# Optimization experiments

Measured on AMD Instinct MI355X. Metric: run time of the kernel, lower is better.

Reference implementation:

```python
import jax, jax.numpy as jnp
import numpy as np

N, H, W = 4, 96, 96
C, G, K = 128, 8, 3
GC = C // G          # group channels = 16
P = K * K            # sampling points per group = 9
PAD = K // 2
OFS = 1.0            # offset_scale
HID = 4 * C          # mlp hidden
EPS = 1e-5           # torch nn.LayerNorm default eps


def _ln(x, g, b):
    m = jnp.mean(x, -1, keepdims=True)
    v = jnp.mean((x - m) ** 2, -1, keepdims=True)
    return (x - m) * jax.lax.rsqrt(v + EPS) * g + b


def _dcnv3_core(x, offset, mask):
    # x: (n,H,W,C) channels-last, offset: (n,H,W,G*P*2), mask: (n,H,W,G,P) softmaxed.
    # Faithful port of dcnv3_core_pytorch (stride=1, dilation=1, zero-pad grid_sample,
    # align_corners=False -> pixel = loc*size - 0.5).
    n = x.shape[0]
    xp = jnp.pad(x, ((0, 0), (PAD, PAD), (PAD, PAD), (0, 0)))
    Hin, Win = H + 2 * PAD, W + 2 * PAD
    L = H * W
    base = (K - 1) // 2 + 0.5
    ref_x = (base + jnp.arange(W, dtype=x.dtype)) / Win  # normalized by padded size
    ref_y = (base + jnp.arange(H, dtype=x.dtype)) / Hin
    k = jnp.arange(K, dtype=x.dtype) - (K - 1) // 2
    dx = jnp.repeat(k, K) / Win  # torch meshgrid('ij'): kernel-x varies slowest
    dy = jnp.tile(k, K) / Hin
    off = offset.reshape(n, H, W, G, P, 2)
    # absolute sampling pixel coords (grid_sample align_corners=False)
    px = (ref_x[None, None, :, None, None] + dx * OFS + off[..., 0] * OFS / Win) * Win - 0.5
    py = (ref_y[None, :, None, None, None] + dy * OFS + off[..., 1] * OFS / Hin) * Hin - 0.5
    # layout (n,G,L,P)
    px = px.transpose(0, 3, 1, 2, 4).reshape(n, G, L, P)
    py = py.transpose(0, 3, 1, 2, 4).reshape(n, G, L, P)
    mk = mask.transpose(0, 3, 1, 2, 4).reshape(n, G, L, P)
    xg = xp.reshape(n, Hin * Win, G, GC).transpose(0, 2, 1, 3)
    x0 = jnp.floor(px); y0 = jnp.floor(py)
    fx = px - x0; fy = py - y0
    x0 = x0.astype(jnp.int32); y0 = y0.astype(jnp.int32)
    x1 = x0 + 1; y1 = y0 + 1
    out = jnp.zeros((n, G, L, GC), x.dtype)
    for yi, xi, w in ((y0, x0, (1 - fy) * (1 - fx)), (y0, x1, (1 - fy) * fx),
                      (y1, x0, fy * (1 - fx)), (y1, x1, fy * fx)):
        valid = (yi >= 0) & (yi < Hin) & (xi >= 0) & (xi < Win)
        idx = jnp.clip(yi, 0, Hin - 1) * Win + jnp.clip(xi, 0, Win - 1)
        v = jnp.take_along_axis(xg, idx.reshape(n, G, L * P, 1), axis=2)
        v = v.reshape(n, G, L, P, GC)
        out = out + jnp.einsum('nglp,nglpc->nglc', jnp.where(valid, w, 0.0) * mk, v)
    return out.transpose(0, 2, 1, 3).reshape(n, H, W, C)


def _dcn(x, w_in, b_in, dw_k, dw_b, dwg, dwb, w_off, b_off, w_msk, b_msk, w_out, b_out):
    n = x.shape[0]
    xproj = x @ w_in + b_in
    x1 = jax.lax.conv_general_dilated(
        x, dw_k, (1, 1), 'SAME',
        dimension_numbers=('NHWC', 'HWIO', 'NHWC'),
        feature_group_count=C) + dw_b
    x1 = jax.nn.gelu(_ln(x1, dwg, dwb), approximate=False)
    offset = x1 @ w_off + b_off
    mask = jax.nn.softmax((x1 @ w_msk + b_msk).reshape(n, H, W, G, P), axis=-1)
    y = _dcnv3_core(xproj, offset, mask)
    return y @ w_out + b_out


def setup_inputs() -> dict:
    key = jax.random.key(0)
    ks = jax.random.split(key, 10)
    rn = lambda k, s, sc: jax.random.normal(k, s, jnp.float32) * sc
    return {
        'x': rn(ks[0], (N, H, W, C), 1.0),
        'ln1g': jnp.ones((C,), jnp.float32), 'ln1b': jnp.zeros((C,), jnp.float32),
        'w_in': rn(ks[1], (C, C), 0.02), 'b_in': jnp.zeros((C,), jnp.float32),
        'dw_k': rn(ks[2], (K, K, 1, C), 0.1), 'dw_b': jnp.zeros((C,), jnp.float32),
        'dwg': jnp.ones((C,), jnp.float32), 'dwb': jnp.zeros((C,), jnp.float32),
        'w_off': rn(ks[3], (C, G * P * 2), 0.01), 'b_off': rn(ks[4], (G * P * 2,), 0.1),
        'w_msk': rn(ks[5], (C, G * P), 0.02), 'b_msk': jnp.zeros((G * P,), jnp.float32),
        'w_out': rn(ks[6], (C, C), 0.02), 'b_out': jnp.zeros((C,), jnp.float32),
        'ln2g': jnp.ones((C,), jnp.float32), 'ln2b': jnp.zeros((C,), jnp.float32),
        'w1': rn(ks[7], (C, HID), 0.02), 'b1': jnp.zeros((HID,), jnp.float32),
        'w2': rn(ks[8], (HID, C), 0.02), 'b2': jnp.zeros((C,), jnp.float32),
    }


def reference(x, ln1g, ln1b, w_in, b_in, dw_k, dw_b, dwg, dwb, w_off, b_off,
              w_msk, b_msk, w_out, b_out, ln2g, ln2b, w1, b1, w2, b2):
    # pre-norm InternImage block: x = x + dcn(LN1(x)); x = x + mlp(LN2(x))
    x = x + _dcn(_ln(x, ln1g, ln1b), w_in, b_in, dw_k, dw_b, dwg, dwb,
                 w_off, b_off, w_msk, b_msk, w_out, b_out)
    h = _ln(x, ln2g, ln2b)
    h = jax.nn.gelu(h @ w1 + b1, approximate=False) @ w2 + b2
    return x + h
```

## Files before the change

### kernel.cpp

```cpp
#include <hip/hip_runtime.h>
#include <hip/hip_bf16.h>
#include <math.h>

using bf16 = __hip_bfloat16;
using bf162 = __hip_bfloat162;

typedef __bf16 bf16x8 __attribute__((ext_vector_type(8)));
typedef float floatx4 __attribute__((ext_vector_type(4)));

constexpr int NB = 4, HH = 96, WW = 96, CC = 128, GG = 8, PP = 9;
constexpr int HW = HH * WW;
constexpr int NPIX = NB * HW;

__device__ __forceinline__ float ld1(const float* p) { return *p; }
__device__ __forceinline__ float ld1(const bf16* p)  { return __bfloat162float(*p); }
__device__ __forceinline__ void st1(float* p, float v) { *p = v; }
__device__ __forceinline__ void st1(bf16* p, float v)  { *p = __float2bfloat16(v); }
__device__ __forceinline__ float b2f(bf16 v) { return __bfloat162float(v); }
__device__ __forceinline__ bf16 f2b(float v) { return __float2bfloat16(v); }
__device__ __forceinline__ float gelu_exact(float v) {
    return 0.5f * v * (1.0f + erff(v * 0.7071067811865475f));
}
__device__ __forceinline__ floatx4 MFMA(bf16x8 a, bf16x8 b, floatx4 c) {
    return __builtin_amdgcn_mfma_f32_16x16x32_bf16(a, b, c, 0, 0, 0);
}

struct PrepArgs {
    const float* src[6];
    bf16* dst[6];
    int K[6], N[6];
    int cum[7];
    const float* b_off; const float* b_msk; float* b_om;
};

__global__ __launch_bounds__(256) void prep_weights(PrepArgs pa, int total)
{
    int t = blockIdx.x * 256 + threadIdx.x;
    if (t >= total) return;
    if (t >= pa.cum[6]) {
        int e = t - pa.cum[6];
        pa.b_om[e] = (e < 144) ? pa.b_off[e] : pa.b_msk[e - 144];
        return;
    }
    int i = 0;
    #pragma unroll
    for (int j = 0; j < 5; ++j) if (t >= pa.cum[j + 1]) i = j + 1;
    int e = t - pa.cum[i];
    int Ki = pa.K[i], Ni = pa.N[i];
    int n = e / Ki, k = e - n * Ki;
    pa.dst[i][e] = f2b(pa.src[i][(size_t)k * Ni + n]);
}

template<typename TI, typename TO>
__global__ __launch_bounds__(256) void ln_kernel(
    const TI* __restrict__ X, const float* __restrict__ g,
    const float* __restrict__ b, TO* __restrict__ out)
{
    int wave = (blockIdx.x * 256 + threadIdx.x) >> 6;
    int lane = threadIdx.x & 63;
    if (wave >= NPIX) return;
    const TI* xp = X + (size_t)wave * 128 + 2 * lane;
    float v0 = ld1(xp), v1 = ld1(xp + 1);
    float s = v0 + v1, q = v0 * v0 + v1 * v1;
    #pragma unroll
    for (int o = 32; o; o >>= 1) { s += __shfl_xor(s, o); q += __shfl_xor(q, o); }
    float mean = s * (1.0f / 128.0f);
    float rstd = rsqrtf(q * (1.0f / 128.0f) - mean * mean + 1e-5f);
    float g0 = g[2 * lane], g1 = g[2 * lane + 1];
    float b0 = b[2 * lane], b1 = b[2 * lane + 1];
    TO* op = out + (size_t)wave * 128 + 2 * lane;
    st1(op,     (v0 - mean) * rstd * g0 + b0);
    st1(op + 1, (v1 - mean) * rstd * g1 + b1);
}

__global__ __launch_bounds__(256) void dwconv_ln_gelu_kernel(
    const bf16* __restrict__ xln, const float* __restrict__ dwk,
    const float* __restrict__ dwb, const float* __restrict__ gam,
    const float* __restrict__ bet, bf16* __restrict__ out)
{
    int wave = (blockIdx.x * 256 + threadIdx.x) >> 6;
    int lane = threadIdx.x & 63;
    if (wave >= NPIX) return;
    int n = wave / HW; int rem = wave % HW;
    int y = rem / WW;  int x = rem % WW;
    const bf162* xp = (const bf162*)xln;
    float a0 = 0.f, a1 = 0.f;
    #pragma unroll
    for (int ky = 0; ky < 3; ++ky) {
        int yy = y + ky - 1;
        if (yy < 0 || yy >= HH) continue;
        #pragma unroll
        for (int kx = 0; kx < 3; ++kx) {
            int xx = x + kx - 1;
            if (xx < 0 || xx >= WW) continue;
            bf162 v = xp[((size_t)(n * HH + yy) * WW + xx) * 64 + lane];
            const float* w = dwk + (ky * 3 + kx) * CC + 2 * lane;
            a0 = fmaf(b2f(v.x), w[0], a0);
            a1 = fmaf(b2f(v.y), w[1], a1);
        }
    }
    a0 += dwb[2 * lane]; a1 += dwb[2 * lane + 1];
    float s = a0 + a1, q = a0 * a0 + a1 * a1;
    #pragma unroll
    for (int o = 32; o; o >>= 1) { s += __shfl_xor(s, o); q += __shfl_xor(q, o); }
    float mean = s * (1.0f / 128.0f);
    float rstd = rsqrtf(q * (1.0f / 128.0f) - mean * mean + 1e-5f);
    float h0 = gelu_exact((a0 - mean) * rstd * gam[2 * lane]     + bet[2 * lane]);
    float h1 = gelu_exact((a1 - mean) * rstd * gam[2 * lane + 1] + bet[2 * lane + 1]);
    bf162 o2; o2.x = f2b(h0); o2.y = f2b(h1);
    ((bf162*)out)[(size_t)wave * 64 + lane] = o2;
}

__global__ __launch_bounds__(256) void dcn_core_kernel(
    const bf16* __restrict__ xproj, const bf16* __restrict__ omr,
    bf16* __restrict__ out)
{
    __shared__ int4   sOff[4][72];
    __shared__ float4 sW[4][72];
    __shared__ float  sRaw[4][72];
    int wv = threadIdx.x >> 6;
    int lane = threadIdx.x & 63;
    int pix = blockIdx.x * 4 + wv;
    int n = pix / HW; int rem = pix % HW;
    int iy = rem / WW; int ix = rem % WW;
    const bf16* om = omr + (size_t)pix * 216;

    for (int e = lane; e < 72; e += 64)
        sRaw[wv][e] = b2f(om[144 + e]);
    __syncthreads();

    for (int e = lane; e < 72; e += 64) {
        int g = e / 9, p = e - 9 * g;
        float mx = -1e30f;
        #pragma unroll
        for (int i = 0; i < 9; ++i) mx = fmaxf(mx, sRaw[wv][g * 9 + i]);
        float ssum = 0.f;
        #pragma unroll
        for (int i = 0; i < 9; ++i) ssum += __expf(sRaw[wv][g * 9 + i] - mx);
        float mw = __expf(sRaw[wv][e] - mx) / ssum;

        float ox = b2f(om[g * 18 + 2 * p]);
        float oy = b2f(om[g * 18 + 2 * p + 1]);
        int kx = p / 3 - 1, ky = p % 3 - 1;
        float px = (float)(ix + kx) + ox;
        float py = (float)(iy + ky) + oy;
        float fx0 = floorf(px), fy0 = floorf(py);
        int x0 = (int)fx0, y0 = (int)fy0;
        float fx = px - fx0, fy = py - fy0;
        bool vx0 = (x0 >= 0) & (x0 < WW), vx1 = (x0 + 1 >= 0) & (x0 + 1 < WW);
        bool vy0 = (y0 >= 0) & (y0 < HH), vy1 = (y0 + 1 >= 0) & (y0 + 1 < HH);
        float w00 = (1.f - fy) * (1.f - fx) * mw * (vy0 && vx0 ? 1.f : 0.f);
        float w01 = (1.f - fy) * fx         * mw * (vy0 && vx1 ? 1.f : 0.f);
        float w10 = fy * (1.f - fx)         * mw * (vy1 && vx0 ? 1.f : 0.f);
        float w11 = fy * fx                 * mw * (vy1 && vx1 ? 1.f : 0.f);
        int x0c = min(max(x0, 0), WW - 1), x1c = min(max(x0 + 1, 0), WW - 1);
        int y0c = min(max(y0, 0), HH - 1), y1c = min(max(y0 + 1, 0), HH - 1);
        sOff[wv][e] = make_int4((y0c * WW + x0c) * CC, (y0c * WW + x1c) * CC,
                                (y1c * WW + x0c) * CC, (y1c * WW + x1c) * CC);
        sW[wv][e] = make_float4(w00, w01, w10, w11);
    }
    __syncthreads();

    const bf16* xb = xproj + (size_t)n * HW * CC + 2 * lane;
    int gbase = (lane >> 3) * 9;
    float a0 = 0.f, a1 = 0.f;
    #pragma unroll
    for (int p = 0; p < 9; ++p) {
        int4 o = sOff[wv][gbase + p];
        float4 w = sW[wv][gbase + p];
        bf162 v00 = *(const bf162*)(xb + o.x);
        bf162 v01 = *(const bf162*)(xb + o.y);
        bf162 v10 = *(const bf162*)(xb + o.z);
        bf162 v11 = *(const bf162*)(xb + o.w);
        a0 += w.x * b2f(v00.x) + w.y * b2f(v01.x) + w.z * b2f(v10.x) + w.w * b2f(v11.x);
        a1 += w.x * b2f(v00.y) + w.y * b2f(v01.y) + w.z * b2f(v10.y) + w.w * b2f(v11.y);
    }
    bf162 o2; o2.x = f2b(a0); o2.y = f2b(a1);
    ((bf162*)out)[(size_t)pix * 64 + lane] = o2;
}

__global__ __launch_bounds__(256) void gemm_mfma_kernel(
    const bf16* __restrict__ A, const bf16* __restrict__ Wt,
    const float* __restrict__ bias, bf16* __restrict__ Out, int M, int Nn, int K)
{
    __shared__ __align__(16) __bf16 As[64][72];
    __shared__ __align__(16) __bf16 Bs[64][72];
    int tid = threadIdx.x;
    int wv = tid >> 6, lane = tid & 63;
    int bm = blockIdx.y * 64, bn = blockIdx.x * 64;
    int mI = lane & 15, q = lane >> 4;
    floatx4 acc[4] = {};

    for (int k0 = 0; k0 < K; k0 += 64) {
        #pragma unroll
        for (int cc = 0; cc < 2; ++cc) {
            int ch = tid * 2 + cc;
            int row = ch >> 3, ko = (ch & 7) * 8;
            *reinterpret_cast<uint4*>(&As[row][ko]) =
                *reinterpret_cast<const uint4*>(A + (size_t)(bm + row) * K + k0 + ko);
            int ng = bn + row;
            uint4 bv = make_uint4(0, 0, 0, 0);
            if (ng < Nn) bv = *reinterpret_cast<const uint4*>(Wt + (size_t)ng * K + k0 + ko);
            *reinterpret_cast<uint4*>(&Bs[row][ko]) = bv;
        }
        __syncthreads();
        #pragma unroll
        for (int kk = 0; kk < 64; kk += 32) {
            bf16x8 a = *reinterpret_cast<const bf16x8*>(&As[wv * 16 + mI][kk + q * 8]);
            #pragma unroll
            for (int t = 0; t < 4; ++t) {
                bf16x8 b = *reinterpret_cast<const bf16x8*>(&Bs[t * 16 + mI][kk + q * 8]);
                acc[t] = MFMA(a, b, acc[t]);
            }
        }
        __syncthreads();
    }
    int row0 = bm + wv * 16 + q * 4;
    #pragma unroll
    for (int t = 0; t < 4; ++t) {
        int col = bn + t * 16 + mI;
        if (col >= Nn) continue;
        float bs = bias[col];
        #pragma unroll
        for (int r = 0; r < 4; ++r)
            st1(Out + (size_t)(row0 + r) * Nn + col, acc[t][r] + bs);
    }
}

__global__ __launch_bounds__(256, 3) void fused_tail_kernel(
    const bf16* __restrict__ ycore, const float* __restrict__ x,
    const bf16* __restrict__ w_outT, const float* __restrict__ b_out,
    const float* __restrict__ ln2g, const float* __restrict__ ln2b,
    const bf16* __restrict__ w1T, const float* __restrict__ b1,
    const bf16* __restrict__ w2T, const float* __restrict__ b2,
    float* __restrict__ out)
{
    __shared__ __align__(16) bf16 sA[64 * 136];
    __shared__ __align__(16) bf16 sXres[64 * 136];
    __shared__ __align__(16) bf16 sH2[64 * 136];
    int tid = threadIdx.x, wv = tid >> 6, lane = tid & 63;
    int mI = lane & 15, q = lane >> 4;
    int bm = blockIdx.x * 64;

    bf16x8 bw0[4][2];
    #pragma unroll
    for (int ks = 0; ks < 4; ++ks)
        #pragma unroll
        for (int ct = 0; ct < 2; ++ct)
            bw0[ks][ct] = *reinterpret_cast<const bf16x8*>(
                w_outT + (size_t)(wv * 32 + ct * 16 + mI) * 128 + ks * 32 + q * 8);

    #pragma unroll
    for (int i = 0; i < 4; ++i) {
        int s = tid + 256 * i;
        int row = s >> 4, ko = (s & 15) * 8;
        *reinterpret_cast<uint4*>(&sA[row * 136 + ko]) =
            *reinterpret_cast<const uint4*>(ycore + (size_t)(bm + row) * 128 + ko);
    }
    __syncthreads();

    floatx4 acc0[4][2] = {};
    #pragma unroll
    for (int ks = 0; ks < 4; ++ks) {
        int k = ks * 32 + q * 8;
        bf16x8 a[4];
        #pragma unroll
        for (int rt = 0; rt < 4; ++rt)
            a[rt] = *reinterpret_cast<const bf16x8*>(&sA[(rt * 16 + mI) * 136 + k]);
        #pragma unroll
        for (int ct = 0; ct < 2; ++ct)
            #pragma unroll
            for (int rt = 0; rt < 4; ++rt)
                acc0[rt][ct] = MFMA(a[rt], bw0[ks][ct], acc0[rt][ct]);
    }
    #pragma unroll
    for (int rt = 0; rt < 4; ++rt)
        #pragma unroll
        for (int ct = 0; ct < 2; ++ct) {
            int col = wv * 32 + ct * 16 + mI;
            float bs = b_out[col];
            #pragma unroll
            for (int r = 0; r < 4; ++r) {
                int row = rt * 16 + q * 4 + r;
                float v = acc0[rt][ct][r] + bs + x[(size_t)(bm + row) * 128 + col];
                sXres[row * 136 + col] = f2b(v);
            }
        }
    __syncthreads();

    {
        int row = tid >> 2, part = tid & 3;
        float s = 0.f, sq = 0.f;
        float vals[32];
        #pragma unroll
        for (int j = 0; j < 4; ++j) {
            bf16x8 v = *reinterpret_cast<const bf16x8*>(&sXres[row * 136 + part * 32 + j * 8]);
            #pragma unroll
            for (int e = 0; e < 8; ++e) {
                float f = (float)v[e];
                vals[j * 8 + e] = f; s += f; sq += f * f;
            }
        }
        s  += __shfl_xor(s, 1);  s += __shfl_xor(s, 2);
        sq += __shfl_xor(sq, 1); sq += __shfl_xor(sq, 2);
        float mean = s * (1.0f / 128.0f);
        float rstd = rsqrtf(sq * (1.0f / 128.0f) - mean * mean + 1e-5f);
        #pragma unroll
        for (int j = 0; j < 4; ++j) {
            bf16x8 o;
            #pragma unroll
            for (int e = 0; e < 8; ++e) {
                int ch = part * 32 + j * 8 + e;
                bf16 t = f2b((vals[j * 8 + e] - mean) * rstd * ln2g[ch] + ln2b[ch]);
                o[e] = *reinterpret_cast<__bf16*>(&t);
            }
            *reinterpret_cast<bf16x8*>(&sH2[row * 136 + part * 32 + j * 8]) = o;
        }
    }
    __syncthreads();

    floatx4 acc2[4][2] = {};
    #pragma unroll 1
    for (int ph = 0; ph < 4; ++ph) {
        bf16x8 bw1[4][2];
        #pragma unroll
        for (int ks = 0; ks < 4; ++ks)
            #pragma unroll
            for (int ct = 0; ct < 2; ++ct)
                bw1[ks][ct] = *reinterpret_cast<const bf16x8*>(
                    w1T + (size_t)(ph * 128 + wv * 32 + ct * 16 + mI) * 128 + ks * 32 + q * 8);
        floatx4 acc1[4][2] = {};
        #pragma unroll
        for (int ks = 0; ks < 4; ++ks) {
            int k = ks * 32 + q * 8;
            bf16x8 a[4];
            #pragma unroll
            for (int rt = 0; rt < 4; ++rt)
                a[rt] = *reinterpret_cast<const bf16x8*>(&sH2[(rt * 16 + mI) * 136 + k]);
            #pragma unroll
            for (int ct = 0; ct < 2; ++ct)
                #pragma unroll
                for (int rt = 0; rt < 4; ++rt)
                    acc1[rt][ct] = MFMA(a[rt], bw1[ks][ct], acc1[rt][ct]);
        }
        __syncthreads();
        bf16x8 bw2[4][2];
        #pragma unroll
        for (int ks = 0; ks < 4; ++ks)
            #pragma unroll
            for (int ct = 0; ct < 2; ++ct)
                bw2[ks][ct] = *reinterpret_cast<const bf16x8*>(
                    w2T + (size_t)(wv * 32 + ct * 16 + mI) * 512 + ph * 128 + ks * 32 + q * 8);
        #pragma unroll
        for (int rt = 0; rt < 4; ++rt)
            #pragma unroll
            for (int ct = 0; ct < 2; ++ct) {
                int lcol = wv * 32 + ct * 16 + mI;
                float bs = b1[ph * 128 + lcol];
                #pragma unroll
                for (int r = 0; r < 4; ++r) {
                    int row = rt * 16 + q * 4 + r;
                    sA[row * 136 + lcol] = f2b(gelu_exact(acc1[rt][ct][r] + bs));
                }
            }
        __syncthreads();
        #pragma unroll
        for (int ks = 0; ks < 4; ++ks) {
            int k = ks * 32 + q * 8;
            bf16x8 a[4];
            #pragma unroll
            for (int rt = 0; rt < 4; ++rt)
                a[rt] = *reinterpret_cast<const bf16x8*>(&sA[(rt * 16 + mI) * 136 + k]);
            #pragma unroll
            for (int ct = 0; ct < 2; ++ct)
                #pragma unroll
                for (int rt = 0; rt < 4; ++rt)
                    acc2[rt][ct] = MFMA(a[rt], bw2[ks][ct], acc2[rt][ct]);
        }
    }
    #pragma unroll
    for (int rt = 0; rt < 4; ++rt)
        #pragma unroll
        for (int ct = 0; ct < 2; ++ct) {
            int col = wv * 32 + ct * 16 + mI;
            float bs = b2[col];
            #pragma unroll
            for (int r = 0; r < 4; ++r) {
                int row = rt * 16 + q * 4 + r;
                out[(size_t)(bm + row) * 128 + col] =
                    acc2[rt][ct][r] + bs + b2f(sXres[row * 136 + col]);
            }
        }
}

extern "C" void kernel_launch(void* const* d_in, const int* in_sizes, int n_in,
                              void* d_out, int out_size, void* d_ws, size_t ws_size,
                              hipStream_t stream)
{
    const float* x     = (const float*)d_in[0];
    const float* ln1g  = (const float*)d_in[1];
    const float* ln1b  = (const float*)d_in[2];
    const float* w_in  = (const float*)d_in[3];
    const float* b_in  = (const float*)d_in[4];
    const float* dw_k  = (const float*)d_in[5];
    const float* dw_b  = (const float*)d_in[6];
    const float* dwg   = (const float*)d_in[7];
    const float* dwb   = (const float*)d_in[8];
    const float* w_off = (const float*)d_in[9];
    const float* b_off = (const float*)d_in[10];
    const float* w_msk = (const float*)d_in[11];
    const float* b_msk = (const float*)d_in[12];
    const float* w_out = (const float*)d_in[13];
    const float* b_out = (const float*)d_in[14];
    const float* ln2g  = (const float*)d_in[15];
    const float* ln2b  = (const float*)d_in[16];
    const float* w1    = (const float*)d_in[17];
    const float* b1    = (const float*)d_in[18];
    const float* w2    = (const float*)d_in[19];
    const float* b2    = (const float*)d_in[20];
    float* out = (float*)d_out;

    bf16* ws = (bf16*)d_ws;
    bf16* xln   = ws;
    bf16* xproj = xln   + (size_t)NPIX * 128;
    bf16* x1    = xproj + (size_t)NPIX * 128;
    bf16* omr   = x1    + (size_t)NPIX * 128;
    bf16* ycore = xln;
    bf16* wT    = ws + (size_t)NPIX * 600;
    bf16* w_inT  = wT;
    bf16* w_omT  = w_inT  + 16384;
    bf16* w_outT = w_omT  + 27648;
    bf16* w1T    = w_outT + 16384;
    bf16* w2T    = w1T    + 65536;
    float* b_om  = (float*)(w2T + 65536);
    const int WTOT = 191488 + 216;

    PrepArgs pa;
    pa.src[0] = w_in;  pa.dst[0] = w_inT;            pa.K[0] = 128; pa.N[0] = 128;
    pa.src[1] = w_off; pa.dst[1] = w_omT;            pa.K[1] = 128; pa.N[1] = 144;
    pa.src[2] = w_msk; pa.dst[2] = w_omT + 144*128;  pa.K[2] = 128; pa.N[2] = 72;
    pa.src[3] = w_out; pa.dst[3] = w_outT;           pa.K[3] = 128; pa.N[3] = 128;
    pa.src[4] = w1;    pa.dst[4] = w1T;              pa.K[4] = 128; pa.N[4] = 512;
    pa.src[5] = w2;    pa.dst[5] = w2T;              pa.K[5] = 512; pa.N[5] = 128;
    pa.cum[0] = 0;     pa.cum[1] = 16384;  pa.cum[2] = 34816; pa.cum[3] = 44032;
    pa.cum[4] = 60416; pa.cum[5] = 125952; pa.cum[6] = 191488;
    pa.b_off = b_off;  pa.b_msk = b_msk;   pa.b_om = b_om;

    const int M = NPIX;
    dim3 blk(256);

    prep_weights<<<(WTOT + 255) / 256, blk, 0, stream>>>(pa, WTOT);
    ln_kernel<float, bf16><<<NPIX / 4, blk, 0, stream>>>(x, ln1g, ln1b, xln);
    gemm_mfma_kernel<<<dim3(2, M / 64), blk, 0, stream>>>(
        xln, w_inT, b_in, xproj, M, 128, 128);
    dwconv_ln_gelu_kernel<<<NPIX / 4, blk, 0, stream>>>(xln, dw_k, dw_b, dwg, dwb, x1);
    gemm_mfma_kernel<<<dim3(4, M / 64), blk, 0, stream>>>(
        x1, w_omT, b_om, omr, M, 216, 128);
    dcn_core_kernel<<<NPIX / 4, blk, 0, stream>>>(xproj, omr, ycore);
    fused_tail_kernel<<<M / 64, blk, 0, stream>>>(
        ycore, x, w_outT, b_out, ln2g, ln2b, w1T, b1, w2T, b2, out);
}
```

Baseline: 236.9 us.

## Replace exact GELU with tanh approximation and keep LN2 residual in registers

Swaps the erf-based GELU for a tanh-form approximation written as a sigmoid with __expf, both in the depthwise-conv kernel and in the MLP tail. In the fused tail kernel the residual is now kept in accumulator registers rather than an LDS buffer. LayerNorm statistics are reduced with shuffles plus a small per-wave partial-sum array, which removes the sXres shared array. Launch bounds go from 3 to 4 blocks per SM to exploit the lower LDS footprint, at the cost of register pressure and a small numerical deviation from exact GELU.

```diff
diff --git a/kernel.cpp b/kernel.cpp
--- a/kernel.cpp
+++ b/kernel.cpp
@@ -18,8 +18,10 @@
 __device__ __forceinline__ void st1(bf16* p, float v)  { *p = __float2bfloat16(v); }
 __device__ __forceinline__ float b2f(bf16 v) { return __bfloat162float(v); }
 __device__ __forceinline__ bf16 f2b(float v) { return __float2bfloat16(v); }
-__device__ __forceinline__ float gelu_exact(float v) {
-    return 0.5f * v * (1.0f + erff(v * 0.7071067811865475f));
+__device__ __forceinline__ float gelu_fast(float v) {
+    float p = v * v;
+    float u2 = v * (-1.5957691216f - 0.0713548162f * p);
+    return v / (1.0f + __expf(u2));
 }
 __device__ __forceinline__ floatx4 MFMA(bf16x8 a, bf16x8 b, floatx4 c) {
     return __builtin_amdgcn_mfma_f32_16x16x32_bf16(a, b, c, 0, 0, 0);
@@ -105,8 +107,8 @@
     for (int o = 32; o; o >>= 1) { s += __shfl_xor(s, o); q += __shfl_xor(q, o); }
     float mean = s * (1.0f / 128.0f);
     float rstd = rsqrtf(q * (1.0f / 128.0f) - mean * mean + 1e-5f);
-    float h0 = gelu_exact((a0 - mean) * rstd * gam[2 * lane]     + bet[2 * lane]);
-    float h1 = gelu_exact((a1 - mean) * rstd * gam[2 * lane + 1] + bet[2 * lane + 1]);
+    float h0 = gelu_fast((a0 - mean) * rstd * gam[2 * lane]     + bet[2 * lane]);
+    float h1 = gelu_fast((a1 - mean) * rstd * gam[2 * lane + 1] + bet[2 * lane + 1]);
     bf162 o2; o2.x = f2b(h0); o2.y = f2b(h1);
     ((bf162*)out)[(size_t)wave * 64 + lane] = o2;
 }
@@ -227,7 +229,7 @@
     }
 }
 
-__global__ __launch_bounds__(256, 3) void fused_tail_kernel(
+__global__ __launch_bounds__(256, 4) void fused_tail_kernel(
     const bf16* __restrict__ ycore, const float* __restrict__ x,
     const bf16* __restrict__ w_outT, const float* __restrict__ b_out,
     const float* __restrict__ ln2g, const float* __restrict__ ln2b,
@@ -236,8 +238,9 @@
     float* __restrict__ out)
 {
     __shared__ __align__(16) bf16 sA[64 * 136];
-    __shared__ __align__(16) bf16 sXres[64 * 136];
     __shared__ __align__(16) bf16 sH2[64 * 136];
+    __shared__ __align__(16) float sPS[64][4];
+    __shared__ __align__(16) float sPQ[64][4];
     int tid = threadIdx.x, wv = tid >> 6, lane = tid & 63;
     int mI = lane & 15, q = lane >> 4;
     int bm = blockIdx.x * 64;
@@ -249,6 +252,12 @@
         for (int ct = 0; ct < 2; ++ct)
             bw0[ks][ct] = *reinterpret_cast<const bf16x8*>(
                 w_outT + (size_t)(wv * 32 + ct * 16 + mI) * 128 + ks * 32 + q * 8);
+    float g2[2], be2[2];
+    #pragma unroll
+    for (int ct = 0; ct < 2; ++ct) {
+        int col = wv * 32 + ct * 16 + mI;
+        g2[ct] = ln2g[col]; be2[ct] = ln2b[col];
+    }
 
     #pragma unroll
     for (int i = 0; i < 4; ++i) {
@@ -274,7 +283,10 @@
                 acc0[rt][ct] = MFMA(a[rt], bw0[ks][ct], acc0[rt][ct]);
     }
     #pragma unroll
-    for (int rt = 0; rt < 4; ++rt)
+    for (int rt = 0; rt < 4; ++rt) {
+        float ps[4], pq[4];
+        #pragma unroll
+        for (int r = 0; r < 4; ++r) { ps[r] = 0.f; pq[r] = 0.f; }
         #pragma unroll
         for (int ct = 0; ct < 2; ++ct) {
             int col = wv * 32 + ct * 16 + mI;
@@ -283,40 +295,42 @@
             for (int r = 0; r < 4; ++r) {
                 int row = rt * 16 + q * 4 + r;
                 float v = acc0[rt][ct][r] + bs + x[(size_t)(bm + row) * 128 + col];
-                sXres[row * 136 + col] = f2b(v);
-            }
-        }
+                v = b2f(f2b(v));
+                acc0[rt][ct][r] = v;
+                ps[r] += v; pq[r] += v * v;
+            }
+        }
+        #pragma unroll
+        for (int r = 0; r < 4; ++r) {
+            #pragma unroll
+            for (int o = 1; o < 16; o <<= 1) {
+                ps[r] += __shfl_xor(ps[r], o);
+                pq[r] += __shfl_xor(pq[r], o);
+            }
+            int row = rt * 16 + q * 4 + r;
+            if (mI == 0) { sPS[row][wv] = ps[r]; sPQ[row][wv] = pq[r]; }
+        }
+    }
     __syncthreads();
 
-    {
-        int row = tid >> 2, part = tid & 3;
-        float s = 0.f, sq = 0.f;
-        float vals[32];
-        #pragma unroll
-        for (int j = 0; j < 4; ++j) {
-            bf16x8 v = *reinterpret_cast<const bf16x8*>(&sXres[row * 136 + part * 32 + j * 8]);
-            #pragma unroll
-            for (int e = 0; e < 8; ++e) {
-                float f = (float)v[e];
-                vals[j * 8 + e] = f; s += f; sq += f * f;
-            }
-        }
-        s  += __shfl_xor(s, 1);  s += __shfl_xor(s, 2);
-        sq += __shfl_xor(sq, 1); sq += __shfl_xor(sq, 2);
-        float mean = s * (1.0f / 128.0f);
-        float rstd = rsqrtf(sq * (1.0f / 128.0f) - mean * mean + 1e-5f);
-        #pragma unroll
-        for (int j = 0; j < 4; ++j) {
-            bf16x8 o;
-            #pragma unroll
-            for (int e = 0; e < 8; ++e) {
-                int ch = part * 32 + j * 8 + e;
-                bf16 t = f2b((vals[j * 8 + e] - mean) * rstd * ln2g[ch] + ln2b[ch]);
-                o[e] = *reinterpret_cast<__bf16*>(&t);
-            }
-            *reinterpret_cast<bf16x8*>(&sH2[row * 136 + part * 32 + j * 8]) = o;
-        }
-    }
+    #pragma unroll
+    for (int rt = 0; rt < 4; ++rt)
+        #pragma unroll
+        for (int r = 0; r < 4; ++r) {
+            int row = rt * 16 + q * 4 + r;
+            float4 s4 = *reinterpret_cast<const float4*>(&sPS[row][0]);
+            float4 q4 = *reinterpret_cast<const float4*>(&sPQ[row][0]);
+            float s = s4.x + s4.y + s4.z + s4.w;
+            float sq = q4.x + q4.y + q4.z + q4.w;
+            float mean = s * (1.0f / 128.0f);
+            float rstd = rsqrtf(sq * (1.0f / 128.0f) - mean * mean + 1e-5f);
+            #pragma unroll
+            for (int ct = 0; ct < 2; ++ct) {
+                int col = wv * 32 + ct * 16 + mI;
+                sH2[row * 136 + col] =
+                    f2b((acc0[rt][ct][r] - mean) * rstd * g2[ct] + be2[ct]);
+            }
+        }
     __syncthreads();
 
     floatx4 acc2[4][2] = {};
@@ -360,7 +374,7 @@
                 #pragma unroll
                 for (int r = 0; r < 4; ++r) {
                     int row = rt * 16 + q * 4 + r;
-                    sA[row * 136 + lcol] = f2b(gelu_exact(acc1[rt][ct][r] + bs));
+                    sA[row * 136 + lcol] = f2b(gelu_fast(acc1[rt][ct][r] + bs));
                 }
             }
         __syncthreads();
@@ -388,7 +402,7 @@
             for (int r = 0; r < 4; ++r) {
                 int row = rt * 16 + q * 4 + r;
                 out[(size_t)(bm + row) * 128 + col] =
-                    acc2[rt][ct][r] + bs + b2f(sXres[row * 136 + col]);
+                    acc2[rt][ct][r] + bs + acc0[rt][ct][r];
             }
         }
 }
```

After: 250.0 us. 5.5% more time.

## Fuse LayerNorm into input-projection GEMM and use tanh-form GELU approximation

Applied to the files above, without the earlier changes.

Removes the standalone LayerNorm kernel and computes LN1 inside the first GEMM's prologue, writing the normalized activations to global for the depthwise conv and also straight into shared memory for the MFMA. The GEMM now loads the full K=128 tile in one pass with a padded 136-stride layout instead of two 64-wide iterations. Exact erf GELU is replaced with a sigmoid-form tanh approximation using __expf in both the dwconv and MLP paths. Both grid.x blocks of the fused kernel redundantly recompute the LayerNorm and store xln twice, and the GELU change alters numerics.

```diff
diff --git a/kernel.cpp b/kernel.cpp
--- a/kernel.cpp
+++ b/kernel.cpp
@@ -18,8 +18,10 @@
 __device__ __forceinline__ void st1(bf16* p, float v)  { *p = __float2bfloat16(v); }
 __device__ __forceinline__ float b2f(bf16 v) { return __bfloat162float(v); }
 __device__ __forceinline__ bf16 f2b(float v) { return __float2bfloat16(v); }
-__device__ __forceinline__ float gelu_exact(float v) {
-    return 0.5f * v * (1.0f + erff(v * 0.7071067811865475f));
+__device__ __forceinline__ float gelu_fast(float v) {
+    float p = v * v;
+    float u2 = v * (-1.5957691216f - 0.0713548162f * p);
+    return v / (1.0f + __expf(u2));
 }
 __device__ __forceinline__ floatx4 MFMA(bf16x8 a, bf16x8 b, floatx4 c) {
     return __builtin_amdgcn_mfma_f32_16x16x32_bf16(a, b, c, 0, 0, 0);
@@ -51,26 +53,89 @@
     pa.dst[i][e] = f2b(pa.src[i][(size_t)k * Ni + n]);
 }
 
-template<typename TI, typename TO>
-__global__ __launch_bounds__(256) void ln_kernel(
-    const TI* __restrict__ X, const float* __restrict__ g,
-    const float* __restrict__ b, TO* __restrict__ out)
-{
-    int wave = (blockIdx.x * 256 + threadIdx.x) >> 6;
-    int lane = threadIdx.x & 63;
-    if (wave >= NPIX) return;
-    const TI* xp = X + (size_t)wave * 128 + 2 * lane;
-    float v0 = ld1(xp), v1 = ld1(xp + 1);
-    float s = v0 + v1, q = v0 * v0 + v1 * v1;
-    #pragma unroll
-    for (int o = 32; o; o >>= 1) { s += __shfl_xor(s, o); q += __shfl_xor(q, o); }
-    float mean = s * (1.0f / 128.0f);
-    float rstd = rsqrtf(q * (1.0f / 128.0f) - mean * mean + 1e-5f);
-    float g0 = g[2 * lane], g1 = g[2 * lane + 1];
-    float b0 = b[2 * lane], b1 = b[2 * lane + 1];
-    TO* op = out + (size_t)wave * 128 + 2 * lane;
-    st1(op,     (v0 - mean) * rstd * g0 + b0);
-    st1(op + 1, (v1 - mean) * rstd * g1 + b1);
+template<bool DOLN>
+__global__ __launch_bounds__(256) void lngemm_kernel(
+    const void* __restrict__ Ain, const bf16* __restrict__ Wt,
+    const float* __restrict__ bias,
+    const float* __restrict__ lng, const float* __restrict__ lnb,
+    bf16* __restrict__ xlnOut,
+    bf16* __restrict__ Out, int Nn)
+{
+    __shared__ __align__(16) bf16 As[64 * 136];
+    __shared__ __align__(16) bf16 Bs[64 * 136];
+    int tid = threadIdx.x, wv = tid >> 6, lane = tid & 63;
+    int mI = lane & 15, q = lane >> 4;
+    int bm = blockIdx.y * 64, bn = blockIdx.x * 64;
+
+    if (DOLN) {
+        int row = tid >> 2, seg = tid & 3;
+        const float* rp = (const float*)Ain + (size_t)(bm + row) * 128 + seg * 32;
+        float v[32]; float s = 0.f, sq = 0.f;
+        #pragma unroll
+        for (int j = 0; j < 8; ++j) {
+            float4 f = *reinterpret_cast<const float4*>(rp + j * 4);
+            v[j*4+0] = f.x; v[j*4+1] = f.y; v[j*4+2] = f.z; v[j*4+3] = f.w;
+            s += f.x + f.y + f.z + f.w;
+            sq += f.x*f.x + f.y*f.y + f.z*f.z + f.w*f.w;
+        }
+        s  += __shfl_xor(s, 1);  s += __shfl_xor(s, 2);
+        sq += __shfl_xor(sq, 1); sq += __shfl_xor(sq, 2);
+        float mean = s * (1.0f / 128.0f);
+        float rstd = rsqrtf(sq * (1.0f / 128.0f) - mean * mean + 1e-5f);
+        bf16x8 o[4];
+        #pragma unroll
+        for (int j = 0; j < 32; ++j) {
+            int ch = seg * 32 + j;
+            bf16 tb = f2b((v[j] - mean) * rstd * lng[ch] + lnb[ch]);
+            o[j >> 3][j & 7] = *reinterpret_cast<__bf16*>(&tb);
+        }
+        #pragma unroll
+        for (int j = 0; j < 4; ++j) {
+            *reinterpret_cast<bf16x8*>(&As[row * 136 + seg * 32 + j * 8]) = o[j];
+            *reinterpret_cast<bf16x8*>(xlnOut + (size_t)(bm + row) * 128 + seg * 32 + j * 8) = o[j];
+        }
+    } else {
+        const bf16* A = (const bf16*)Ain;
+        #pragma unroll
+        for (int i = 0; i < 4; ++i) {
+            int sI = tid + 256 * i;
+            int row = sI >> 4, ko = (sI & 15) * 8;
+            *reinterpret_cast<uint4*>(&As[row * 136 + ko]) =
+                *reinterpret_cast<const uint4*>(A + (size_t)(bm + row) * 128 + ko);
+        }
+    }
+    #pragma unroll
+    for (int i = 0; i < 4; ++i) {
+        int sI = tid + 256 * i;
+        int row = sI >> 4, ko = (sI & 15) * 8;
+        int ng = bn + row;
+        uint4 bv = make_uint4(0, 0, 0, 0);
+        if (ng < Nn) bv = *reinterpret_cast<const uint4*>(Wt + (size_t)ng * 128 + ko);
+        *reinterpret_cast<uint4*>(&Bs[row * 136 + ko]) = bv;
+    }
+    __syncthreads();
+
+    floatx4 acc[4] = {};
+    #pragma unroll
+    for (int kk = 0; kk < 4; ++kk) {
+        int k = kk * 32 + q * 8;
+        bf16x8 a = *reinterpret_cast<const bf16x8*>(&As[(wv * 16 + mI) * 136 + k]);
+        #pragma unroll
+        for (int t = 0; t < 4; ++t) {
+            bf16x8 b = *reinterpret_cast<const bf16x8*>(&Bs[(t * 16 + mI) * 136 + k]);
+            acc[t] = MFMA(a, b, acc[t]);
+        }
+    }
+    int row0 = bm + wv * 16 + q * 4;
+    #pragma unroll
+    for (int t = 0; t < 4; ++t) {
+        int col = bn + t * 16 + mI;
+        if (col >= Nn) continue;
+        float bs = bias[col];
+        #pragma unroll
+        for (int r = 0; r < 4; ++r)
+            st1(Out + (size_t)(row0 + r) * Nn + col, acc[t][r] + bs);
+    }
 }
 
 __global__ __launch_bounds__(256) void dwconv_ln_gelu_kernel(
@@ -105,8 +170,8 @@
     for (int o = 32; o; o >>= 1) { s += __shfl_xor(s, o); q += __shfl_xor(q, o); }
     float mean = s * (1.0f / 128.0f);
     float rstd = rsqrtf(q * (1.0f / 128.0f) - mean * mean + 1e-5f);
-    float h0 = gelu_exact((a0 - mean) * rstd * gam[2 * lane]     + bet[2 * lane]);
-    float h1 = gelu_exact((a1 - mean) * rstd * gam[2 * lane + 1] + bet[2 * lane + 1]);
+    float h0 = gelu_fast((a0 - mean) * rstd * gam[2 * lane]     + bet[2 * lane]);
+    float h1 = gelu_fast((a1 - mean) * rstd * gam[2 * lane + 1] + bet[2 * lane + 1]);
     bf162 o2; o2.x = f2b(h0); o2.y = f2b(h1);
     ((bf162*)out)[(size_t)wave * 64 + lane] = o2;
 }
@@ -179,54 +244,6 @@
     ((bf162*)out)[(size_t)pix * 64 + lane] = o2;
 }
 
-__global__ __launch_bounds__(256) void gemm_mfma_kernel(
-    const bf16* __restrict__ A, const bf16* __restrict__ Wt,
-    const float* __restrict__ bias, bf16* __restrict__ Out, int M, int Nn, int K)
-{
-    __shared__ __align__(16) __bf16 As[64][72];
-    __shared__ __align__(16) __bf16 Bs[64][72];
-    int tid = threadIdx.x;
-    int wv = tid >> 6, lane = tid & 63;
-    int bm = blockIdx.y * 64, bn = blockIdx.x * 64;
-    int mI = lane & 15, q = lane >> 4;
-    floatx4 acc[4] = {};
-
-    for (int k0 = 0; k0 < K; k0 += 64) {
-        #pragma unroll
-        for (int cc = 0; cc < 2; ++cc) {
-            int ch = tid * 2 + cc;
-            int row = ch >> 3, ko = (ch & 7) * 8;
-            *reinterpret_cast<uint4*>(&As[row][ko]) =
-                *reinterpret_cast<const uint4*>(A + (size_t)(bm + row) * K + k0 + ko);
-            int ng = bn + row;
-            uint4 bv = make_uint4(0, 0, 0, 0);
-            if (ng < Nn) bv = *reinterpret_cast<const uint4*>(Wt + (size_t)ng * K + k0 + ko);
-            *reinterpret_cast<uint4*>(&Bs[row][ko]) = bv;
-        }
-        __syncthreads();
-        #pragma unroll
-        for (int kk = 0; kk < 64; kk += 32) {
-            bf16x8 a = *reinterpret_cast<const bf16x8*>(&As[wv * 16 + mI][kk + q * 8]);
-            #pragma unroll
-            for (int t = 0; t < 4; ++t) {
-                bf16x8 b = *reinterpret_cast<const bf16x8*>(&Bs[t * 16 + mI][kk + q * 8]);
-                acc[t] = MFMA(a, b, acc[t]);
-            }
-        }
-        __syncthreads();
-    }
-    int row0 = bm + wv * 16 + q * 4;
-    #pragma unroll
-    for (int t = 0; t < 4; ++t) {
-        int col = bn + t * 16 + mI;
-        if (col >= Nn) continue;
-        float bs = bias[col];
-        #pragma unroll
-        for (int r = 0; r < 4; ++r)
-            st1(Out + (size_t)(row0 + r) * Nn + col, acc[t][r] + bs);
-    }
-}
-
 __global__ __launch_bounds__(256, 3) void fused_tail_kernel(
     const bf16* __restrict__ ycore, const float* __restrict__ x,
     const bf16* __restrict__ w_outT, const float* __restrict__ b_out,
@@ -360,7 +377,7 @@
                 #pragma unroll
                 for (int r = 0; r < 4; ++r) {
                     int row = rt * 16 + q * 4 + r;
-                    sA[row * 136 + lcol] = f2b(gelu_exact(acc1[rt][ct][r] + bs));
+                    sA[row * 136 + lcol] = f2b(gelu_fast(acc1[rt][ct][r] + bs));
                 }
             }
         __syncthreads();
@@ -450,12 +467,11 @@
     dim3 blk(256);
 
     prep_weights<<<(WTOT + 255) / 256, blk, 0, stream>>>(pa, WTOT);
-    ln_kernel<float, bf16><<<NPIX / 4, blk, 0, stream>>>(x, ln1g, ln1b, xln);
-    gemm_mfma_kernel<<<dim3(2, M / 64), blk, 0, stream>>>(
-        xln, w_inT, b_in, xproj, M, 128, 128);
+    lngemm_kernel<true><<<dim3(2, M / 64), blk, 0, stream>>>(
+        x, w_inT, b_in, ln1g, ln1b, xln, xproj, 128);
     dwconv_ln_gelu_kernel<<<NPIX / 4, blk, 0, stream>>>(xln, dw_k, dw_b, dwg, dwb, x1);
-    gemm_mfma_kernel<<<dim3(4, M / 64), blk, 0, stream>>>(
-        x1, w_omT, b_om, omr, M, 216, 128);
+    lngemm_kernel<false><<<dim3(4, M / 64), blk, 0, stream>>>(
+        x1, w_omT, b_om, nullptr, nullptr, nullptr, omr, 216);
     dcn_core_kernel<<<NPIX / 4, blk, 0, stream>>>(xproj, omr, ycore);
     fused_tail_kernel<<<M / 64, blk, 0, stream>>>(
         ycore, x, w_outT, b_out, ln2g, ln2b, w1T, b1, w2T, b2, out);
```

After: 252.1 us. +6.4%, slower.
